# Optimization experiments

Measured on AMD Instinct MI355X. Metric: run time of the kernel, lower is better.

## Reference

```python
import jax, jax.numpy as jnp
import numpy as np

NUM_CLASSES = 80
BBOX_W, OBJ_W, CLS_W = 2.0, 1.0, 0.5
ALPHA, GAMMA = 0.25, 2.0


def setup_inputs() -> dict:
    key = jax.random.key(0)
    ks = jax.random.split(key, 8)
    B, T = 32, 64
    return {
        "cls_p4": jax.random.normal(ks[0], (B, 1 + NUM_CLASSES, 80, 80), jnp.float32),
        "reg_p4": jax.random.normal(ks[1], (B, 4, 80, 80), jnp.float32),
        "cls_p5": jax.random.normal(ks[2], (B, 1 + NUM_CLASSES, 40, 40), jnp.float32),
        "reg_p5": jax.random.normal(ks[3], (B, 4, 40, 40), jnp.float32),
        "t4_cls": jax.random.randint(ks[4], (B, T), 0, NUM_CLASSES, jnp.int32),
        "t4_box": jax.random.uniform(ks[5], (B, T, 4), jnp.float32),
        "t4_mask": jnp.ones((B, T), jnp.float32),
        "t5_cls": jax.random.randint(ks[6], (B, T), 0, NUM_CLASSES, jnp.int32),
        "t5_box": jax.random.uniform(ks[7], (B, T, 4), jnp.float32),
        "t5_mask": jnp.ones((B, T), jnp.float32),
    }


def _bce_logits(x, t):
    # stable BCEWithLogits: log(1+e^x) - x*t
    return jnp.logaddexp(0.0, x) - x * t


def _scale_loss(cls_p, reg_p, cls_ids, box, mask):
    B, C, H, W = cls_p.shape
    tx = box[..., 0] * W  # [B,T]
    ty = box[..., 1] * H
    tw = box[..., 2] * W
    th = box[..., 3] * H
    gx = jnp.clip(tx, 0, W - 1).astype(jnp.int32)
    gy = jnp.clip(ty, 0, H - 1).astype(jnp.int32)
    bb = jnp.arange(B)[:, None]  # [B,1] broadcast over T

    # gather per-target reg/cls vectors: [B,T,4] and [B,T,C]
    rv = jnp.transpose(reg_p, (0, 2, 3, 1))[bb, gy, gx]
    cv = jnp.transpose(cls_p, (0, 2, 3, 1))[bb, gy, gx]

    dx = jax.nn.sigmoid(rv[..., 0])
    dy = jax.nn.sigmoid(rv[..., 1])
    dw = jnp.exp(jnp.clip(rv[..., 2], -4.0, 4.0))
    dh = jnp.exp(jnp.clip(rv[..., 3], -4.0, 4.0))
    px = gx.astype(jnp.float32) + dx
    py = gy.astype(jnp.float32) + dy
    pred_box = jnp.stack([px - dw / 2, py - dh / 2, px + dw / 2, py + dh / 2], -1)
    tgt_box = jnp.stack([tx - tw / 2, ty - th / 2, tx + tw / 2, ty + th / 2], -1)

    d = pred_box - tgt_box
    sl1 = jnp.where(jnp.abs(d) < 1.0, 0.5 * d * d, jnp.abs(d) - 0.5).mean(-1)  # [B,T]
    lb = (sl1 * mask).sum()

    # objectness loss at target cells (target = 1)
    obj_t = cv[..., 0]
    lo = (jax.nn.softplus(-obj_t) * mask).sum()

    # focal classification loss
    onehot = jax.nn.one_hot(cls_ids, C - 1, dtype=cls_p.dtype)  # [B,T,NC]
    logits = cv[..., 1:]
    bce = _bce_logits(logits, onehot)
    p = jax.nn.sigmoid(logits)
    pt = p * onehot + (1.0 - p) * (1.0 - onehot)
    focal = (ALPHA * (1.0 - pt) ** GAMMA * bce).mean(-1)  # [B,T]
    lc = (focal * mask).sum()

    n = mask.sum()

    # background objectness: cells not hit by any valid target
    obj_map = jnp.zeros((B, H, W), cls_p.dtype).at[bb, gy, gx].max(mask)
    bg = obj_map == 0
    bg_cnt = bg.sum()
    bce_bg = jnp.where(bg, jax.nn.softplus(cls_p[:, 0]), 0.0).sum()
    lo = lo + 0.05 * jnp.where(bg_cnt > 0, bce_bg / jnp.maximum(bg_cnt, 1), 0.0)
    return lb, lo, lc, n


def reference(cls_p4, reg_p4, cls_p5, reg_p5,
              t4_cls, t4_box, t4_mask, t5_cls, t5_box, t5_mask):
    lb4, lo4, lc4, n4 = _scale_loss(cls_p4, reg_p4, t4_cls, t4_box, t4_mask)
    lb5, lo5, lc5, n5 = _scale_loss(cls_p5, reg_p5, t5_cls, t5_box, t5_mask)
    lb, lo, lc, n = lb4 + lb5, lo4 + lo5, lc4 + lc5, n4 + n5
    lb = jnp.where(n > 0, lb / jnp.maximum(n, 1), lb)
    lc = jnp.where(n > 0, lc / jnp.maximum(n, 1), lc)
    lo = lo / jnp.maximum(n, 1.0)
    total = BBOX_W * lb + OBJ_W * lo + CLS_W * lc
    return total
```

## Files before the change

### kernel.cpp

```cpp
#include <hip/hip_runtime.h>
#include <math.h>

#define NUM_CLASSES 80
#define C_CH (NUM_CLASSES + 1)

__device__ __forceinline__ float softplusf(float x) {
    return fmaxf(x, 0.f) + log1pf(expf(-fabsf(x)));
}
__device__ __forceinline__ float sigmoidf_(float x) {
    return 1.f / (1.f + expf(-x));
}


__global__ void target_kernel(
    const float* __restrict__ cls_p4, const float* __restrict__ reg_p4,
    const float* __restrict__ cls_p5, const float* __restrict__ reg_p5,
    const int* __restrict__ t4_cls, const float* __restrict__ t4_box, const float* __restrict__ t4_mask,
    const int* __restrict__ t5_cls, const float* __restrict__ t5_box, const float* __restrict__ t5_mask,
    float* __restrict__ tpart, unsigned int* __restrict__ flags4, unsigned int* __restrict__ flags5,
    int B, int T)
{
    const int BT = B * T;
    const int wave = threadIdx.x >> 6;
    const int lane = threadIdx.x & 63;
    const int tg = blockIdx.x * 4 + wave;

    float lb = 0.f, lo = 0.f, lcv = 0.f, msum = 0.f;

    if (tg < 2 * BT) {
        const int scale = (tg >= BT) ? 1 : 0;
        const int ti = scale ? tg - BT : tg;
        const int b = ti / T;

        const float* cls_p; const float* reg_p; const int* tc; const float* tb_; const float* tm;
        unsigned int* flags; int H, W;
        if (!scale) { cls_p = cls_p4; reg_p = reg_p4; tc = t4_cls; tb_ = t4_box; tm = t4_mask; flags = flags4; H = 80; W = 80; }
        else        { cls_p = cls_p5; reg_p = reg_p5; tc = t5_cls; tb_ = t5_box; tm = t5_mask; flags = flags5; H = 40; W = 40; }
        const int HW = H * W;

        const float mask = tm[ti];
        const int   cid  = tc[ti];
        const float bx0 = tb_[ti * 4 + 0], bx1 = tb_[ti * 4 + 1];
        const float bx2 = tb_[ti * 4 + 2], bx3 = tb_[ti * 4 + 3];

        const float tx = bx0 * (float)W, ty = bx1 * (float)H;
        const float tw = bx2 * (float)W, th = bx3 * (float)H;
        const int gx = (int)fminf(fmaxf(tx, 0.f), (float)(W - 1));
        const int gy = (int)fminf(fmaxf(ty, 0.f), (float)(H - 1));
        const int cell = gy * W + gx;

        if (lane == 0 && mask > 0.f) {
            int gidx = b * HW + cell;
            atomicOr(&flags[gidx >> 5], 1u << (gidx & 31));
        }

        const float* cvbase = cls_p + (size_t)b * C_CH * HW + cell;

        float rvq = 0.f;
        if (lane < 4) rvq = reg_p[(size_t)(b * 4 + lane) * HW + cell];
        float objq = (lane == 0) ? cvbase[0] : 0.f;

        float fsum = 0.f;
        for (int c = lane; c < NUM_CLASSES; c += 64) {
            float x   = cvbase[(size_t)(c + 1) * HW];
            float tgt = (c == cid) ? 1.f : 0.f;
            float bce = softplusf(x) - x * tgt;
            float p   = sigmoidf_(x);
            float pt  = p * tgt + (1.f - p) * (1.f - tgt);
            float om  = 1.f - pt;
            fsum += 0.25f * om * om * bce;
        }
        for (int off = 32; off > 0; off >>= 1) fsum += __shfl_down(fsum, off, 64);

        float rv0 = __shfl(rvq, 0, 64), rv1 = __shfl(rvq, 1, 64);
        float rv2 = __shfl(rvq, 2, 64), rv3 = __shfl(rvq, 3, 64);

        if (lane == 0) {
            lcv = (fsum * (1.f / (float)NUM_CLASSES)) * mask;
            lo  = softplusf(-objq) * mask;

            float dx = sigmoidf_(rv0), dy = sigmoidf_(rv1);
            float dw = expf(fminf(fmaxf(rv2, -4.f), 4.f));
            float dh = expf(fminf(fmaxf(rv3, -4.f), 4.f));
            float px = (float)gx + dx, py = (float)gy + dy;
            float pb0 = px - dw * 0.5f, pb1 = py - dh * 0.5f, pb2 = px + dw * 0.5f, pb3 = py + dh * 0.5f;
            float tb0 = tx - tw * 0.5f, tb1 = ty - th * 0.5f, tb2 = tx + tw * 0.5f, tb3 = ty + th * 0.5f;
            float s = 0.f, d, a;
            d = pb0 - tb0; a = fabsf(d); s += (a < 1.f) ? 0.5f * d * d : a - 0.5f;
            d = pb1 - tb1; a = fabsf(d); s += (a < 1.f) ? 0.5f * d * d : a - 0.5f;
            d = pb2 - tb2; a = fabsf(d); s += (a < 1.f) ? 0.5f * d * d : a - 0.5f;
            d = pb3 - tb3; a = fabsf(d); s += (a < 1.f) ? 0.5f * d * d : a - 0.5f;
            lb = (s * 0.25f) * mask;
            msum = mask;
        }
    }

    __shared__ float s4[4][4];
    if (lane == 0) { s4[wave][0] = lb; s4[wave][1] = lo; s4[wave][2] = lcv; s4[wave][3] = msum; }
    __syncthreads();
    if (threadIdx.x < 4) {
        float v = s4[0][threadIdx.x] + s4[1][threadIdx.x] + s4[2][threadIdx.x] + s4[3][threadIdx.x];
        tpart[blockIdx.x * 4 + threadIdx.x] = v;
    }
}

__global__ void bg_kernel(
    const float* __restrict__ cls_p4, const float* __restrict__ cls_p5,
    const unsigned int* __restrict__ flags4, const unsigned int* __restrict__ flags5,
    float* __restrict__ bgpart4, float* __restrict__ bgpart5, int nb4)
{
    const int blk = blockIdx.x;
    const int tid = threadIdx.x;
    float sp = 0.f, cnt = 0.f;
    int scale, oblk;
    if (blk < nb4) {
        scale = 0; oblk = blk;
        int b = blk / 25, j = blk - b * 25;
        int cell = j * 256 + tid;
        int gidx = b * 6400 + cell;
        unsigned int w = flags4[gidx >> 5];
        if (!((w >> (gidx & 31)) & 1u)) {
            sp = softplusf(cls_p4[(size_t)b * (C_CH * 6400) + cell]);
            cnt = 1.f;
        }
    } else {
        scale = 1; oblk = blk - nb4;
        int b = oblk / 7, j = oblk - b * 7;
        int cell = j * 256 + tid;
        if (cell < 1600) {
            int gidx = b * 1600 + cell;
            unsigned int w = flags5[gidx >> 5];
            if (!((w >> (gidx & 31)) & 1u)) {
                sp = softplusf(cls_p5[(size_t)b * (C_CH * 1600) + cell]);
                cnt = 1.f;
            }
        }
    }
    for (int off = 32; off > 0; off >>= 1) {
        sp  += __shfl_down(sp,  off, 64);
        cnt += __shfl_down(cnt, off, 64);
    }
    __shared__ float ss[4][2];
    const int wid = tid >> 6;
    if ((tid & 63) == 0) { ss[wid][0] = sp; ss[wid][1] = cnt; }
    __syncthreads();
    if (tid == 0) {
        float a = ss[0][0] + ss[1][0] + ss[2][0] + ss[3][0];
        float c = ss[0][1] + ss[1][1] + ss[2][1] + ss[3][1];
        float* o = scale ? bgpart5 : bgpart4;
        o[oblk * 2]     = a;
        o[oblk * 2 + 1] = c;
    }
}

__global__ void final_kernel(
    const float* __restrict__ tpart, int nT,
    const float* __restrict__ bgpart4, int nb4,
    const float* __restrict__ bgpart5, int nb5,
    float* __restrict__ out)
{
    float lb = 0.f, lo = 0.f, lc = 0.f, n = 0.f, b4 = 0.f, c4 = 0.f, b5 = 0.f, c5 = 0.f;
    for (int i = threadIdx.x; i < nT; i += 256) {
        lb += tpart[i * 4 + 0]; lo += tpart[i * 4 + 1];
        lc += tpart[i * 4 + 2]; n  += tpart[i * 4 + 3];
    }
    for (int i = threadIdx.x; i < nb4; i += 256) { b4 += bgpart4[2 * i]; c4 += bgpart4[2 * i + 1]; }
    for (int i = threadIdx.x; i < nb5; i += 256) { b5 += bgpart5[2 * i]; c5 += bgpart5[2 * i + 1]; }

    __shared__ float sbuf[4];
    float vals[8] = { lb, lo, lc, n, b4, c4, b5, c5 };
    float tot[8];
    for (int k = 0; k < 8; k++) {
        float v = vals[k];
        for (int off = 32; off > 0; off >>= 1) v += __shfl_down(v, off, 64);
        __syncthreads();
        if ((threadIdx.x & 63) == 0) sbuf[threadIdx.x >> 6] = v;
        __syncthreads();
        tot[k] = sbuf[0] + sbuf[1] + sbuf[2] + sbuf[3];
    }
    if (threadIdx.x == 0) {
        float lbt = tot[0], lot = tot[1], lct = tot[2], nt = tot[3];
        lot += 0.05f * ((tot[5] > 0.f) ? tot[4] / fmaxf(tot[5], 1.f) : 0.f);
        lot += 0.05f * ((tot[7] > 0.f) ? tot[6] / fmaxf(tot[7], 1.f) : 0.f);
        float nd = fmaxf(nt, 1.f);
        if (nt > 0.f) { lbt /= nd; lct /= nd; }
        lot /= fmaxf(nt, 1.f);
        out[0] = 2.0f * lbt + 1.0f * lot + 0.5f * lct;
    }
}

extern "C" void kernel_launch(void* const* d_in, const int* in_sizes, int n_in,
                              void* d_out, int out_size, void* d_ws, size_t ws_size,
                              hipStream_t stream) {
    const float* cls_p4 = (const float*)d_in[0];
    const float* reg_p4 = (const float*)d_in[1];
    const float* cls_p5 = (const float*)d_in[2];
    const float* reg_p5 = (const float*)d_in[3];
    const int*   t4_cls = (const int*)d_in[4];
    const float* t4_box = (const float*)d_in[5];
    const float* t4_mask= (const float*)d_in[6];
    const int*   t5_cls = (const int*)d_in[7];
    const float* t5_box = (const float*)d_in[8];
    const float* t5_mask= (const float*)d_in[9];

    const int B = in_sizes[0] / (C_CH * 6400);
    const int T = in_sizes[4] / B;
    const int BT = B * T;

    const int fw4 = (B * 6400 + 31) / 32;
    const int fw5 = (B * 1600 + 31) / 32;
    unsigned int* flags4 = (unsigned int*)d_ws;
    unsigned int* flags5 = flags4 + fw4;
    float* tpart = (float*)(flags5 + fw5);
    const int nTblk = (2 * BT + 3) / 4;
    float* bgpart4 = tpart + (size_t)nTblk * 4;
    const int nb4 = B * 25;
    float* bgpart5 = bgpart4 + (size_t)nb4 * 2;
    const int nb5 = B * 7;

    hipMemsetAsync(d_ws, 0, (size_t)(fw4 + fw5) * sizeof(unsigned int), stream);

    target_kernel<<<nTblk, 256, 0, stream>>>(
        cls_p4, reg_p4, cls_p5, reg_p5,
        t4_cls, t4_box, t4_mask, t5_cls, t5_box, t5_mask,
        tpart, flags4, flags5, B, T);

    bg_kernel<<<nb4 + nb5, 256, 0, stream>>>(cls_p4, cls_p5, flags4, flags5,
                                             bgpart4, bgpart5, nb4);

    final_kernel<<<1, 256, 0, stream>>>(tpart, nTblk, bgpart4, nb4, bgpart5, nb5,
                                        (float*)d_out);
}
```

Measured before the change: 131.7 us.

## Fuse target and background passes; subtract occupied cells via shared-memory hash

```diff
diff --git a/kernel.cpp b/kernel.cpp
--- a/kernel.cpp
+++ b/kernel.cpp
@@ -12,18 +12,43 @@
 }
 
 
-__global__ void target_kernel(
+__global__ void fused_kernel(
     const float* __restrict__ cls_p4, const float* __restrict__ reg_p4,
     const float* __restrict__ cls_p5, const float* __restrict__ reg_p5,
     const int* __restrict__ t4_cls, const float* __restrict__ t4_box, const float* __restrict__ t4_mask,
     const int* __restrict__ t5_cls, const float* __restrict__ t5_box, const float* __restrict__ t5_mask,
-    float* __restrict__ tpart, unsigned int* __restrict__ flags4, unsigned int* __restrict__ flags5,
-    int B, int T)
+    float* __restrict__ bgpart, float* __restrict__ tpart,
+    int B, int T, int nbg4, int nbg5)
 {
+    const int tid = threadIdx.x;
+    const int nbg = nbg4 + nbg5;
+
+    if ((int)blockIdx.x < nbg) {
+        const int blk = blockIdx.x;
+        float sp = 0.f;
+        if (blk < nbg4) {
+            int b = blk / 25, j = blk - b * 25;
+            int cell = j * 256 + tid;
+            sp = softplusf(cls_p4[(size_t)b * (C_CH * 6400) + cell]);
+        } else {
+            int o = blk - nbg4;
+            int b = o / 7, j = o - b * 7;
+            int cell = j * 256 + tid;
+            if (cell < 1600)
+                sp = softplusf(cls_p5[(size_t)b * (C_CH * 1600) + cell]);
+        }
+        for (int off = 32; off > 0; off >>= 1) sp += __shfl_down(sp, off, 64);
+        __shared__ float ss[4];
+        if ((tid & 63) == 0) ss[tid >> 6] = sp;
+        __syncthreads();
+        if (tid == 0) bgpart[blockIdx.x] = ss[0] + ss[1] + ss[2] + ss[3];
+        return;
+    }
+
     const int BT = B * T;
-    const int wave = threadIdx.x >> 6;
-    const int lane = threadIdx.x & 63;
-    const int tg = blockIdx.x * 4 + wave;
+    const int wave = tid >> 6;
+    const int lane = tid & 63;
+    const int tg = ((int)blockIdx.x - nbg) * 4 + wave;
 
     float lb = 0.f, lo = 0.f, lcv = 0.f, msum = 0.f;
 
@@ -33,9 +58,9 @@
         const int b = ti / T;
 
         const float* cls_p; const float* reg_p; const int* tc; const float* tb_; const float* tm;
-        unsigned int* flags; int H, W;
-        if (!scale) { cls_p = cls_p4; reg_p = reg_p4; tc = t4_cls; tb_ = t4_box; tm = t4_mask; flags = flags4; H = 80; W = 80; }
-        else        { cls_p = cls_p5; reg_p = reg_p5; tc = t5_cls; tb_ = t5_box; tm = t5_mask; flags = flags5; H = 40; W = 40; }
+        int H, W;
+        if (!scale) { cls_p = cls_p4; reg_p = reg_p4; tc = t4_cls; tb_ = t4_box; tm = t4_mask; H = 80; W = 80; }
+        else        { cls_p = cls_p5; reg_p = reg_p5; tc = t5_cls; tb_ = t5_box; tm = t5_mask; H = 40; W = 40; }
         const int HW = H * W;
 
         const float mask = tm[ti];
@@ -48,11 +73,6 @@
         const int gx = (int)fminf(fmaxf(tx, 0.f), (float)(W - 1));
         const int gy = (int)fminf(fmaxf(ty, 0.f), (float)(H - 1));
         const int cell = gy * W + gx;
-
-        if (lane == 0 && mask > 0.f) {
-            int gidx = b * HW + cell;
-            atomicOr(&flags[gidx >> 5], 1u << (gidx & 31));
-        }
 
         const float* cvbase = cls_p + (size_t)b * C_CH * HW + cell;
 
@@ -98,90 +118,100 @@
     __shared__ float s4[4][4];
     if (lane == 0) { s4[wave][0] = lb; s4[wave][1] = lo; s4[wave][2] = lcv; s4[wave][3] = msum; }
     __syncthreads();
-    if (threadIdx.x < 4) {
-        float v = s4[0][threadIdx.x] + s4[1][threadIdx.x] + s4[2][threadIdx.x] + s4[3][threadIdx.x];
-        tpart[blockIdx.x * 4 + threadIdx.x] = v;
-    }
-}
-
-__global__ void bg_kernel(
+    if (tid < 4) {
+        float v = s4[0][tid] + s4[1][tid] + s4[2][tid] + s4[3][tid];
+        tpart[((int)blockIdx.x - nbg) * 4 + tid] = v;
+    }
+}
+
+#define HASH_SZ 8192
+
+__global__ void __launch_bounds__(1024) final_kernel(
     const float* __restrict__ cls_p4, const float* __restrict__ cls_p5,
-    const unsigned int* __restrict__ flags4, const unsigned int* __restrict__ flags5,
-    float* __restrict__ bgpart4, float* __restrict__ bgpart5, int nb4)
+    const float* __restrict__ t4_box, const float* __restrict__ t4_mask,
+    const float* __restrict__ t5_box, const float* __restrict__ t5_mask,
+    const float* __restrict__ bgpart, int nbg4, int nbg5,
+    const float* __restrict__ tpart, int nT4,
+    int B, int T, float* __restrict__ out)
 {
-    const int blk = blockIdx.x;
+    __shared__ unsigned int hash[HASH_SZ];
+    __shared__ float red[16][12];
     const int tid = threadIdx.x;
-    float sp = 0.f, cnt = 0.f;
-    int scale, oblk;
-    if (blk < nb4) {
-        scale = 0; oblk = blk;
-        int b = blk / 25, j = blk - b * 25;
-        int cell = j * 256 + tid;
-        int gidx = b * 6400 + cell;
-        unsigned int w = flags4[gidx >> 5];
-        if (!((w >> (gidx & 31)) & 1u)) {
-            sp = softplusf(cls_p4[(size_t)b * (C_CH * 6400) + cell]);
-            cnt = 1.f;
-        }
-    } else {
-        scale = 1; oblk = blk - nb4;
-        int b = oblk / 7, j = oblk - b * 7;
-        int cell = j * 256 + tid;
-        if (cell < 1600) {
-            int gidx = b * 1600 + cell;
-            unsigned int w = flags5[gidx >> 5];
-            if (!((w >> (gidx & 31)) & 1u)) {
-                sp = softplusf(cls_p5[(size_t)b * (C_CH * 1600) + cell]);
-                cnt = 1.f;
+    const int BT = B * T;
+
+    for (int i = tid; i < HASH_SZ; i += 1024) hash[i] = 0u;
+    __syncthreads();
+
+    float occ_sp4 = 0.f, occ_c4 = 0.f, occ_sp5 = 0.f, occ_c5 = 0.f;
+    for (int g = tid; g < 2 * BT; g += 1024) {
+        const int scale = (g >= BT) ? 1 : 0;
+        const int ti = scale ? g - BT : g;
+        const float* tb_ = scale ? t5_box : t4_box;
+        const float* tm  = scale ? t5_mask : t4_mask;
+        const float mask = tm[ti];
+        if (mask > 0.f) {
+            const int b = ti / T;
+            const int W = scale ? 40 : 80, H = W;
+            const int HW = W * H;
+            const float tx = tb_[ti * 4 + 0] * (float)W;
+            const float ty = tb_[ti * 4 + 1] * (float)H;
+            const int gx = (int)fminf(fmaxf(tx, 0.f), (float)(W - 1));
+            const int gy = (int)fminf(fmaxf(ty, 0.f), (float)(H - 1));
+            const int cell = gy * W + gx;
+            const unsigned int id = ((unsigned)scale << 18) | (unsigned)(b * HW + cell);
+            const unsigned int key = id + 1u;
+            unsigned int h = (id * 2654435761u) >> 19;
+            h &= (HASH_SZ - 1);
+            for (;;) {
+                unsigned int old = atomicCAS(&hash[h], 0u, key);
+                if (old == 0u) {
+                    const float* cls_p = scale ? cls_p5 : cls_p4;
+                    float sp = softplusf(cls_p[(size_t)b * C_CH * HW + cell]);
+                    if (scale) { occ_sp5 += sp; occ_c5 += 1.f; }
+                    else       { occ_sp4 += sp; occ_c4 += 1.f; }
+                    break;
+                }
+                if (old == key) break;
+                h = (h + 1) & (HASH_SZ - 1);
             }
         }
     }
-    for (int off = 32; off > 0; off >>= 1) {
-        sp  += __shfl_down(sp,  off, 64);
-        cnt += __shfl_down(cnt, off, 64);
-    }
-    __shared__ float ss[4][2];
-    const int wid = tid >> 6;
-    if ((tid & 63) == 0) { ss[wid][0] = sp; ss[wid][1] = cnt; }
+
+    float lb = 0.f, lo = 0.f, lc = 0.f, n = 0.f, bg4 = 0.f, bg5 = 0.f;
+    for (int i = tid; i < nT4; i += 1024) {
+        lb += tpart[i * 4 + 0]; lo += tpart[i * 4 + 1];
+        lc += tpart[i * 4 + 2]; n  += tpart[i * 4 + 3];
+    }
+    for (int i = tid; i < nbg4; i += 1024) bg4 += bgpart[i];
+    for (int i = tid; i < nbg5; i += 1024) bg5 += bgpart[nbg4 + i];
+
+    float vals[10] = { lb, lo, lc, n, bg4, bg5, occ_sp4, occ_c4, occ_sp5, occ_c5 };
+    #pragma unroll
+    for (int k = 0; k < 10; k++) {
+        float v = vals[k];
+        for (int off = 32; off > 0; off >>= 1) v += __shfl_down(v, off, 64);
+        vals[k] = v;
+    }
+    if ((tid & 63) == 0) {
+        #pragma unroll
+        for (int k = 0; k < 10; k++) red[tid >> 6][k] = vals[k];
+    }
     __syncthreads();
     if (tid == 0) {
-        float a = ss[0][0] + ss[1][0] + ss[2][0] + ss[3][0];
-        float c = ss[0][1] + ss[1][1] + ss[2][1] + ss[3][1];
-        float* o = scale ? bgpart5 : bgpart4;
-        o[oblk * 2]     = a;
-        o[oblk * 2 + 1] = c;
-    }
-}
-
-__global__ void final_kernel(
-    const float* __restrict__ tpart, int nT,
-    const float* __restrict__ bgpart4, int nb4,
-    const float* __restrict__ bgpart5, int nb5,
-    float* __restrict__ out)
-{
-    float lb = 0.f, lo = 0.f, lc = 0.f, n = 0.f, b4 = 0.f, c4 = 0.f, b5 = 0.f, c5 = 0.f;
-    for (int i = threadIdx.x; i < nT; i += 256) {
-        lb += tpart[i * 4 + 0]; lo += tpart[i * 4 + 1];
-        lc += tpart[i * 4 + 2]; n  += tpart[i * 4 + 3];
-    }
-    for (int i = threadIdx.x; i < nb4; i += 256) { b4 += bgpart4[2 * i]; c4 += bgpart4[2 * i + 1]; }
-    for (int i = threadIdx.x; i < nb5; i += 256) { b5 += bgpart5[2 * i]; c5 += bgpart5[2 * i + 1]; }
-
-    __shared__ float sbuf[4];
-    float vals[8] = { lb, lo, lc, n, b4, c4, b5, c5 };
-    float tot[8];
-    for (int k = 0; k < 8; k++) {
-        float v = vals[k];
-        for (int off = 32; off > 0; off >>= 1) v += __shfl_down(v, off, 64);
-        __syncthreads();
-        if ((threadIdx.x & 63) == 0) sbuf[threadIdx.x >> 6] = v;
-        __syncthreads();
-        tot[k] = sbuf[0] + sbuf[1] + sbuf[2] + sbuf[3];
-    }
-    if (threadIdx.x == 0) {
-        float lbt = tot[0], lot = tot[1], lct = tot[2], nt = tot[3];
-        lot += 0.05f * ((tot[5] > 0.f) ? tot[4] / fmaxf(tot[5], 1.f) : 0.f);
-        lot += 0.05f * ((tot[7] > 0.f) ? tot[6] / fmaxf(tot[7], 1.f) : 0.f);
+        float t[10];
+        #pragma unroll
+        for (int k = 0; k < 10; k++) {
+            float s = 0.f;
+            for (int w = 0; w < 16; w++) s += red[w][k];
+            t[k] = s;
+        }
+        float lbt = t[0], lot = t[1], lct = t[2], nt = t[3];
+        float bce_bg4 = t[4] - t[6];
+        float bce_bg5 = t[5] - t[8];
+        float cnt4 = (float)(B * 6400) - t[7];
+        float cnt5 = (float)(B * 1600) - t[9];
+        lot += 0.05f * ((cnt4 > 0.f) ? bce_bg4 / fmaxf(cnt4, 1.f) : 0.f);
+        lot += 0.05f * ((cnt5 > 0.f) ? bce_bg5 / fmaxf(cnt5, 1.f) : 0.f);
         float nd = fmaxf(nt, 1.f);
         if (nt > 0.f) { lbt /= nd; lct /= nd; }
         lot /= fmaxf(nt, 1.f);
@@ -207,27 +237,19 @@
     const int T = in_sizes[4] / B;
     const int BT = B * T;
 
-    const int fw4 = (B * 6400 + 31) / 32;
-    const int fw5 = (B * 1600 + 31) / 32;
-    unsigned int* flags4 = (unsigned int*)d_ws;
-    unsigned int* flags5 = flags4 + fw4;
-    float* tpart = (float*)(flags5 + fw5);
+    const int nbg4 = B * 25;
+    const int nbg5 = B * 7;
     const int nTblk = (2 * BT + 3) / 4;
-    float* bgpart4 = tpart + (size_t)nTblk * 4;
-    const int nb4 = B * 25;
-    float* bgpart5 = bgpart4 + (size_t)nb4 * 2;
-    const int nb5 = B * 7;
-
-    hipMemsetAsync(d_ws, 0, (size_t)(fw4 + fw5) * sizeof(unsigned int), stream);
-
-    target_kernel<<<nTblk, 256, 0, stream>>>(
+
+    float* bgpart = (float*)d_ws;
+    float* tpart  = bgpart + (nbg4 + nbg5);
+
+    fused_kernel<<<nbg4 + nbg5 + nTblk, 256, 0, stream>>>(
         cls_p4, reg_p4, cls_p5, reg_p5,
         t4_cls, t4_box, t4_mask, t5_cls, t5_box, t5_mask,
-        tpart, flags4, flags5, B, T);
-
-    bg_kernel<<<nb4 + nb5, 256, 0, stream>>>(cls_p4, cls_p5, flags4, flags5,
-                                             bgpart4, bgpart5, nb4);
-
-    final_kernel<<<1, 256, 0, stream>>>(tpart, nTblk, bgpart4, nb4, bgpart5, nb5,
-                                        (float*)d_out);
-}
+        bgpart, tpart, B, T, nbg4, nbg5);
+
+    final_kernel<<<1, 1024, 0, stream>>>(
+        cls_p4, cls_p5, t4_box, t4_mask, t5_box, t5_mask,
+        bgpart, nbg4, nbg5, tpart, nTblk, B, T, (float*)d_out);
+}
```

Result: slower. 148.0 us (+12.4%).
